# Performance work log

Hardware: AMD Instinct MI355X
Metric: run time of the kernel (lower is better)

The kernel has to match this reference:

```python
import jax, jax.numpy as jnp
import numpy as np

# dims
B, T = 32, 512            # batch (cells), num TFs
G, PPG = 2000, 10         # num genes, cCRE peaks per gene (uniform cut)
P = G * PPG               # total peaks = 20000
E = 64000                 # PPI edges
NOUT = 10                 # output channels
GENE_DIM = 2              # GCNConv out dim


def setup_inputs() -> dict:
    key = jax.random.key(0)
    ks = jax.random.split(key, 8)
    x = jax.random.normal(ks[0], (B, T, P), jnp.float32)
    edge_index = jax.random.randint(ks[1], (2, E), 0, G, dtype=jnp.int32)
    # concatenation of all per-gene subNet fc1 weights: gene i uses W_sub[:, cut[i]:cut[i+1]]
    W_sub = jax.random.normal(ks[2], (T, P), jnp.float32) * 0.01
    b_sub = jnp.zeros((G,), jnp.float32)
    # PyG GCNConv lin.weight has shape [out=2, in=1]
    W_gcn = jax.random.normal(ks[3], (GENE_DIM, 1), jnp.float32)
    b_gcn = jnp.zeros((GENE_DIM,), jnp.float32)
    W_out = jax.random.normal(ks[4], (NOUT, G * GENE_DIM), jnp.float32) * 0.01
    b_out = jnp.zeros((NOUT,), jnp.float32)
    return dict(x=x, edge_index=edge_index, W_sub=W_sub, b_sub=b_sub,
                W_gcn=W_gcn, b_gcn=b_gcn, W_out=W_out, b_out=b_out)


def reference(x, edge_index, W_sub, b_sub, W_gcn, b_gcn, W_out, b_out):
    gene_seg = jnp.arange(P) // PPG  # peak -> gene id (uniform cut list)
    # block-diagonal tiny-FC loop fused: per-gene Linear(num_peak*num_tf -> 1)
    per_peak = jnp.einsum('btp,tp->bp', x, W_sub)                  # [B, P]
    h = jax.ops.segment_sum(per_peak.T, gene_seg, num_segments=G).T + b_sub  # [B, G]
    h = jax.nn.relu(h)                                              # cat_activate
    # GCNConv(1 -> 2), add_self_loops=False: xw = h W^T, then D^-1/2 A D^-1/2 agg
    xw = h[:, :, None] * W_gcn[:, 0][None, None, :]                # [B, G, 2]
    row, col = edge_index[0], edge_index[1]
    deg = jax.ops.segment_sum(jnp.ones((E,), x.dtype), col, num_segments=G)
    dinv = jnp.where(deg > 0, deg ** -0.5, 0.0)
    norm = dinv[row] * dinv[col]                                   # [E]
    msg = xw[:, row, :] * norm[None, :, None]                      # [B, E, 2]
    agg = jax.ops.segment_sum(msg.transpose(1, 0, 2), col,
                              num_segments=G).transpose(1, 0, 2) + b_gcn  # [B, G, 2]
    g = jax.nn.relu(agg).reshape(B, G * GENE_DIM)
    return g @ W_out.T + b_out                                     # [B, NOUT]
```

## Files before the change

kernel.cpp:

```cpp
#include <hip/hip_runtime.h>
#include <math.h>

#define BN    32
#define TN    512
#define GN    2000
#define PPGN  10
#define PN    (GN*PPGN)
#define EN    64000
#define NOUTN 10
#define PQN   (PN/4)

#define TCH   8
#define TPC   (TN/TCH)
#define BQ    4
#define BPH   (BN/BQ)

typedef float float4v __attribute__((ext_vector_type(4)));

__global__ __launch_bounds__(256)
void k_perpeak(const float* __restrict__ x,
               const float* __restrict__ W_sub,
               float* __restrict__ partial) {
    int ptile = blockIdx.x;
    int bq    = blockIdx.y;
    int tc    = blockIdx.z;
    int pq    = ptile * 256 + threadIdx.x;
    if (pq >= PQN) return;
    int b0 = bq * BPH;
    int t0 = tc * TPC;

    const float4v* xp = (const float4v*)x + ((size_t)b0 * TN + t0) * PQN + pq;
    const float4v* wp = (const float4v*)W_sub + (size_t)t0 * PQN + pq;

    float4v acc[BPH];
#pragma unroll
    for (int j = 0; j < BPH; ++j) acc[j] = (float4v){0.f, 0.f, 0.f, 0.f};

#pragma unroll 2
    for (int t = 0; t < TPC; ++t) {
        float4v wv = wp[(size_t)t * PQN];
#pragma unroll
        for (int j = 0; j < BPH; ++j) {
            float4v xv = __builtin_nontemporal_load(xp + ((size_t)j * TN + t) * PQN);
            acc[j] = xv * wv + acc[j];
        }
    }

    float4v* pp = (float4v*)partial + ((size_t)tc * BN + b0) * PQN + pq;
#pragma unroll
    for (int j = 0; j < BPH; ++j)
        __builtin_nontemporal_store(acc[j], pp + (size_t)j * PQN);
}

__global__ void k_h(const float* __restrict__ partial,
                    const float* __restrict__ b_sub,
                    float* __restrict__ h) {
    int idx = blockIdx.x * blockDim.x + threadIdx.x;
    if (idx >= BN * GN) return;
    int g = idx % GN, b = idx / GN;
    float s = b_sub[g];
    for (int tc = 0; tc < TCH; ++tc) {
        const float* pp = partial + ((size_t)tc * BN + b) * PN + g * PPGN;
#pragma unroll
        for (int k = 0; k < PPGN; ++k) s += pp[k];
    }
    h[idx] = fmaxf(s, 0.0f);
}

__global__ void k_deg(const int* __restrict__ col, float* __restrict__ deg) {
    int e = blockIdx.x * blockDim.x + threadIdx.x;
    if (e < EN) atomicAdd(&deg[col[e]], 1.0f);
}

__global__ void k_dinv(const float* __restrict__ deg, float* __restrict__ dinv) {
    int g = blockIdx.x * blockDim.x + threadIdx.x;
    if (g < GN) {
        float d = deg[g];
        dinv[g] = (d > 0.0f) ? (1.0f / sqrtf(d)) : 0.0f;
    }
}

__global__ __launch_bounds__(256)
void k_s(const int* __restrict__ row, const int* __restrict__ col,
         const float* __restrict__ dinv, const float* __restrict__ h,
         float* __restrict__ s) {
    __shared__ float s_lds[GN];
    int b = blockIdx.x;
    for (int g = threadIdx.x; g < GN; g += 256) s_lds[g] = 0.0f;
    __syncthreads();
    const float* hb = h + (size_t)b * GN;
    for (int e = threadIdx.x; e < EN; e += 256) {
        int r = row[e], c = col[e];
        float nrm = dinv[r] * dinv[c];
        atomicAdd(&s_lds[c], nrm * hb[r]);
    }
    __syncthreads();
    for (int g = threadIdx.x; g < GN; g += 256)
        s[(size_t)b * GN + g] = s_lds[g];
}

__global__ void k_out(const float* __restrict__ s,
                      const float* __restrict__ W_gcn,
                      const float* __restrict__ b_gcn,
                      const float* __restrict__ W_out,
                      const float* __restrict__ b_out,
                      float* __restrict__ out) {
    int b = blockIdx.x / NOUTN;
    int n = blockIdx.x % NOUTN;
    int lane = threadIdx.x;

    float w0 = W_gcn[0], w1 = W_gcn[1];
    float c0 = b_gcn[0], c1 = b_gcn[1];

    float acc = 0.0f;
    for (int g = lane; g < GN; g += 64) {
        float sv = s[(size_t)b * GN + g];
        float g0 = fmaxf(fmaf(sv, w0, c0), 0.0f);
        float g1 = fmaxf(fmaf(sv, w1, c1), 0.0f);
        const float* wo = &W_out[(size_t)n * (GN * 2) + 2 * g];
        acc = fmaf(g0, wo[0], acc);
        acc = fmaf(g1, wo[1], acc);
    }
#pragma unroll
    for (int off = 32; off > 0; off >>= 1)
        acc += __shfl_down(acc, off);
    if (lane == 0) out[b * NOUTN + n] = acc + b_out[n];
}

extern "C" void kernel_launch(void* const* d_in, const int* in_sizes, int n_in,
                              void* d_out, int out_size, void* d_ws, size_t ws_size,
                              hipStream_t stream) {
    const float* x         = (const float*)d_in[0];
    const int*   edge_index= (const int*)  d_in[1];
    const float* W_sub     = (const float*)d_in[2];
    const float* b_sub     = (const float*)d_in[3];
    const float* W_gcn     = (const float*)d_in[4];
    const float* b_gcn     = (const float*)d_in[5];
    const float* W_out     = (const float*)d_in[6];
    const float* b_out     = (const float*)d_in[7];
    float* out = (float*)d_out;

    char* ws = (char*)d_ws;
    float* partial = (float*)(ws);
    float* h       = (float*)(ws + 20480000);
    float* deg     = (float*)(ws + 20736000);
    float* dinv    = (float*)(ws + 20744000);
    float* s       = (float*)(ws + 20752000);

    const int* row = edge_index;
    const int* col = edge_index + EN;

    hipMemsetAsync(deg, 0, GN * sizeof(float), stream);

    dim3 grid_pp(20, BQ, TCH);
    k_perpeak<<<grid_pp, 256, 0, stream>>>(x, W_sub, partial);
    k_h      <<<((BN * GN) + 255) / 256, 256, 0, stream>>>(partial, b_sub, h);
    k_deg    <<<(EN + 255) / 256,        256, 0, stream>>>(col, deg);
    k_dinv   <<<(GN + 255) / 256,        256, 0, stream>>>(deg, dinv);
    k_s      <<<BN, 256, 0, stream>>>(row, col, dinv, h, s);
    k_out    <<<BN * NOUTN, 64, 0, stream>>>(s, W_gcn, b_gcn, W_out, b_out, out);
}
```

Before: 359.1 us.

## Remap per-peak kernel to one block per batch and TF chunk

The per-peak reduction kernel now has one 512-thread block per (batch, TF-chunk) pair, and each thread covers up to 10 peak-quads across the full peak range. Before, each thread held 8 batches and reused one W_sub load across them. The new mapping streams x contiguously per block but reloads W_sub once for every batch, relying on L2 to absorb the repeats. The grid shrinks to 256 blocks, which may limit memory-level parallelism on this GPU.

```diff
diff --git a/kernel.cpp b/kernel.cpp
--- a/kernel.cpp
+++ b/kernel.cpp
@@ -12,44 +12,47 @@
 
 #define TCH   8
 #define TPC   (TN/TCH)
-#define BQ    4
-#define BPH   (BN/BQ)
+#define NK    10
 
 typedef float float4v __attribute__((ext_vector_type(4)));
 
-__global__ __launch_bounds__(256)
+__global__ __launch_bounds__(512)
 void k_perpeak(const float* __restrict__ x,
                const float* __restrict__ W_sub,
                float* __restrict__ partial) {
-    int ptile = blockIdx.x;
-    int bq    = blockIdx.y;
-    int tc    = blockIdx.z;
-    int pq    = ptile * 256 + threadIdx.x;
-    if (pq >= PQN) return;
-    int b0 = bq * BPH;
+    int b  = blockIdx.x;
+    int tc = blockIdx.y;
     int t0 = tc * TPC;
 
-    const float4v* xp = (const float4v*)x + ((size_t)b0 * TN + t0) * PQN + pq;
-    const float4v* wp = (const float4v*)W_sub + (size_t)t0 * PQN + pq;
+    const float4v* xp = (const float4v*)x + ((size_t)b * TN + t0) * PQN;
+    const float4v* wp = (const float4v*)W_sub + (size_t)t0 * PQN;
 
-    float4v acc[BPH];
+    float4v acc[NK];
 #pragma unroll
-    for (int j = 0; j < BPH; ++j) acc[j] = (float4v){0.f, 0.f, 0.f, 0.f};
+    for (int k = 0; k < NK; ++k) acc[k] = (float4v){0.f, 0.f, 0.f, 0.f};
 
-#pragma unroll 2
+#pragma unroll 1
     for (int t = 0; t < TPC; ++t) {
-        float4v wv = wp[(size_t)t * PQN];
+        const float4v* xr = xp + (size_t)t * PQN;
+        const float4v* wr = wp + (size_t)t * PQN;
 #pragma unroll
-        for (int j = 0; j < BPH; ++j) {
-            float4v xv = __builtin_nontemporal_load(xp + ((size_t)j * TN + t) * PQN);
-            acc[j] = xv * wv + acc[j];
+        for (int k = 0; k < NK; ++k) {
+            int p = (int)threadIdx.x + 512 * k;
+            if (p < PQN) {
+                float4v xv = __builtin_nontemporal_load(xr + p);
+                float4v wv = wr[p];
+                acc[k] = xv * wv + acc[k];
+            }
         }
     }
 
-    float4v* pp = (float4v*)partial + ((size_t)tc * BN + b0) * PQN + pq;
+    float4v* pp = (float4v*)partial + ((size_t)tc * BN + b) * PQN;
 #pragma unroll
-    for (int j = 0; j < BPH; ++j)
-        __builtin_nontemporal_store(acc[j], pp + (size_t)j * PQN);
+    for (int k = 0; k < NK; ++k) {
+        int p = (int)threadIdx.x + 512 * k;
+        if (p < PQN)
+            __builtin_nontemporal_store(acc[k], pp + p);
+    }
 }
 
 __global__ void k_h(const float* __restrict__ partial,
@@ -152,8 +155,8 @@
 
     hipMemsetAsync(deg, 0, GN * sizeof(float), stream);
 
-    dim3 grid_pp(20, BQ, TCH);
-    k_perpeak<<<grid_pp, 256, 0, stream>>>(x, W_sub, partial);
+    dim3 grid_pp(BN, TCH);
+    k_perpeak<<<grid_pp, 512, 0, stream>>>(x, W_sub, partial);
     k_h      <<<((BN * GN) + 255) / 256, 256, 0, stream>>>(partial, b_sub, h);
     k_deg    <<<(EN + 255) / 256,        256, 0, stream>>>(col, deg);
     k_dinv   <<<(GN + 255) / 256,        256, 0, stream>>>(deg, dinv);
```

Result: slower. 398.4 us (+10.9%).

## Fuse degree, normalization, GCN aggregation and output GEMV into one kernel

Applied to the files above, without the earlier changes.

Replaces the memset plus four small kernels (degree, dinv, scatter, output projection) with one per-batch kernel that computes degree and dinv in LDS, scatters messages into LDS, and does the final projection from LDS. This removes several launches and global round-trips for deg/dinv/s. In exchange, each of the 32 blocks redundantly recomputes the degree over all 64000 edges, and the output GEMV now runs on only 32 blocks instead of 320.

```diff
diff --git a/kernel.cpp b/kernel.cpp
--- a/kernel.cpp
+++ b/kernel.cpp
@@ -67,64 +67,59 @@
     h[idx] = fmaxf(s, 0.0f);
 }
 
-__global__ void k_deg(const int* __restrict__ col, float* __restrict__ deg) {
-    int e = blockIdx.x * blockDim.x + threadIdx.x;
-    if (e < EN) atomicAdd(&deg[col[e]], 1.0f);
-}
+__global__ __launch_bounds__(256)
+void k_epi(const int* __restrict__ row, const int* __restrict__ col,
+           const float* __restrict__ h,
+           const float* __restrict__ W_gcn, const float* __restrict__ b_gcn,
+           const float* __restrict__ W_out, const float* __restrict__ b_out,
+           float* __restrict__ out) {
+    __shared__ float dinv_l[GN];
+    __shared__ float h_l[GN];
+    __shared__ float s_l[GN];
+    int b = blockIdx.x;
 
-__global__ void k_dinv(const float* __restrict__ deg, float* __restrict__ dinv) {
-    int g = blockIdx.x * blockDim.x + threadIdx.x;
-    if (g < GN) {
-        float d = deg[g];
-        dinv[g] = (d > 0.0f) ? (1.0f / sqrtf(d)) : 0.0f;
+    for (int g = threadIdx.x; g < GN; g += 256) {
+        dinv_l[g] = 0.0f;
+        s_l[g]    = 0.0f;
+        h_l[g]    = h[(size_t)b * GN + g];
     }
-}
+    __syncthreads();
 
-__global__ __launch_bounds__(256)
-void k_s(const int* __restrict__ row, const int* __restrict__ col,
-         const float* __restrict__ dinv, const float* __restrict__ h,
-         float* __restrict__ s) {
-    __shared__ float s_lds[GN];
-    int b = blockIdx.x;
-    for (int g = threadIdx.x; g < GN; g += 256) s_lds[g] = 0.0f;
+    for (int e = threadIdx.x; e < EN; e += 256)
+        atomicAdd(&dinv_l[col[e]], 1.0f);
     __syncthreads();
-    const float* hb = h + (size_t)b * GN;
+
+    for (int g = threadIdx.x; g < GN; g += 256) {
+        float d = dinv_l[g];
+        dinv_l[g] = (d > 0.0f) ? (1.0f / sqrtf(d)) : 0.0f;
+    }
+    __syncthreads();
+
     for (int e = threadIdx.x; e < EN; e += 256) {
         int r = row[e], c = col[e];
-        float nrm = dinv[r] * dinv[c];
-        atomicAdd(&s_lds[c], nrm * hb[r]);
+        atomicAdd(&s_l[c], dinv_l[r] * dinv_l[c] * h_l[r]);
     }
     __syncthreads();
-    for (int g = threadIdx.x; g < GN; g += 256)
-        s[(size_t)b * GN + g] = s_lds[g];
-}
 
-__global__ void k_out(const float* __restrict__ s,
-                      const float* __restrict__ W_gcn,
-                      const float* __restrict__ b_gcn,
-                      const float* __restrict__ W_out,
-                      const float* __restrict__ b_out,
-                      float* __restrict__ out) {
-    int b = blockIdx.x / NOUTN;
-    int n = blockIdx.x % NOUTN;
-    int lane = threadIdx.x;
-
+    int wave = threadIdx.x >> 6;
+    int lane = threadIdx.x & 63;
     float w0 = W_gcn[0], w1 = W_gcn[1];
     float c0 = b_gcn[0], c1 = b_gcn[1];
-
-    float acc = 0.0f;
-    for (int g = lane; g < GN; g += 64) {
-        float sv = s[(size_t)b * GN + g];
-        float g0 = fmaxf(fmaf(sv, w0, c0), 0.0f);
-        float g1 = fmaxf(fmaf(sv, w1, c1), 0.0f);
-        const float* wo = &W_out[(size_t)n * (GN * 2) + 2 * g];
-        acc = fmaf(g0, wo[0], acc);
-        acc = fmaf(g1, wo[1], acc);
+    for (int n = wave; n < NOUTN; n += 4) {
+        float acc = 0.0f;
+        for (int g = lane; g < GN; g += 64) {
+            float sv = s_l[g];
+            float g0 = fmaxf(fmaf(sv, w0, c0), 0.0f);
+            float g1 = fmaxf(fmaf(sv, w1, c1), 0.0f);
+            const float* wo = &W_out[(size_t)n * (GN * 2) + 2 * g];
+            acc = fmaf(g0, wo[0], acc);
+            acc = fmaf(g1, wo[1], acc);
+        }
+#pragma unroll
+        for (int off = 32; off > 0; off >>= 1)
+            acc += __shfl_down(acc, off);
+        if (lane == 0) out[b * NOUTN + n] = acc + b_out[n];
     }
-#pragma unroll
-    for (int off = 32; off > 0; off >>= 1)
-        acc += __shfl_down(acc, off);
-    if (lane == 0) out[b * NOUTN + n] = acc + b_out[n];
 }
 
 extern "C" void kernel_launch(void* const* d_in, const int* in_sizes, int n_in,
@@ -143,20 +138,12 @@
     char* ws = (char*)d_ws;
     float* partial = (float*)(ws);
     float* h       = (float*)(ws + 20480000);
-    float* deg     = (float*)(ws + 20736000);
-    float* dinv    = (float*)(ws + 20744000);
-    float* s       = (float*)(ws + 20752000);
 
     const int* row = edge_index;
     const int* col = edge_index + EN;
 
-    hipMemsetAsync(deg, 0, GN * sizeof(float), stream);
-
     dim3 grid_pp(20, BQ, TCH);
     k_perpeak<<<grid_pp, 256, 0, stream>>>(x, W_sub, partial);
     k_h      <<<((BN * GN) + 255) / 256, 256, 0, stream>>>(partial, b_sub, h);
-    k_deg    <<<(EN + 255) / 256,        256, 0, stream>>>(col, deg);
-    k_dinv   <<<(GN + 255) / 256,        256, 0, stream>>>(deg, dinv);
-    k_s      <<<BN, 256, 0, stream>>>(row, col, dinv, h, s);
-    k_out    <<<BN * NOUTN, 64, 0, stream>>>(s, W_gcn, b_gcn, W_out, b_out, out);
+    k_epi    <<<BN, 256, 0, stream>>>(row, col, h, W_gcn, b_gcn, W_out, b_out, out);
 }
```

New measurement: 415.9 us. 1.16x slower.
